# Performance work log

Measured on AMD Instinct MI355X. Metric: run time of the kernel, lower is better.

Reference implementation:

```python
import jax, jax.numpy as jnp
import numpy as np

HID = 4096; H = 128; P = 64; N = 128; G = 8; K = 4; CH = 128
INTER = H * P                      # 8192
CONV_DIM = INTER + 2 * G * N       # 10240
PROJ = INTER + CONV_DIM + H        # 18560
EPS = 1e-5


def segsum(x):
    # stable segment-sum: out[..., i, j] = sum_{j < k <= i} x[..., k]; -inf above diagonal
    T = x.shape[-1]
    xe = jnp.repeat(x[..., None], T, axis=-1)          # [..., i, j] = x[..., i]
    strict = jnp.tril(jnp.ones((T, T), bool), -1)
    s = jnp.cumsum(jnp.where(strict, xe, 0.0), axis=-2)
    keep = jnp.tril(jnp.ones((T, T), bool), 0)
    return jnp.where(keep, s, -jnp.inf)


def setup_inputs() -> dict:
    key = jax.random.key(0)
    ks = jax.random.split(key, 6)
    b, L = 2, 2048
    hidden_states = jax.random.normal(ks[0], (b, L, HID), jnp.float32)
    in_proj_w = jax.random.normal(ks[1], (PROJ, HID), jnp.float32) * (HID ** -0.5)
    conv_w = jax.random.normal(ks[2], (CONV_DIM, 1, K), jnp.float32) * 0.2
    conv_b = jax.random.normal(ks[3], (CONV_DIM,), jnp.float32) * 0.02
    dt_bias = jnp.ones((H,), jnp.float32)
    A_log = jnp.log(jnp.arange(1, H + 1, dtype=jnp.float32))
    D = jnp.ones((H,), jnp.float32)
    norm_weight = jnp.ones((INTER,), jnp.float32)
    out_proj_w = jax.random.normal(ks[4], (HID, INTER), jnp.float32) * (INTER ** -0.5)
    return dict(hidden_states=hidden_states, in_proj_w=in_proj_w, conv_w=conv_w, conv_b=conv_b,
                dt_bias=dt_bias, A_log=A_log, D=D, norm_weight=norm_weight, out_proj_w=out_proj_w)


def _mamba2(hidden_states, in_proj_w, conv_w, conv_b, dt_bias, A_log, D, norm_weight, out_proj_w):
    b, L, _ = hidden_states.shape
    nchunk = L // CH  # seq_len chosen to be a multiple of chunk_size (pad_size = 0)

    # in_proj and split into gate | conv path (x,B,C) | dt
    proj = hidden_states @ in_proj_w.T
    gate, hBC, dt = jnp.split(proj, [INTER, INTER + CONV_DIM], axis=-1)

    # causal depthwise conv1d (padding k-1, truncate) + SiLU
    xp = jnp.pad(hBC.transpose(0, 2, 1), ((0, 0), (0, 0), (K - 1, 0)))
    xc = jax.lax.conv_general_dilated(xp, conv_w, (1,), 'VALID',
                                      feature_group_count=CONV_DIM,
                                      dimension_numbers=('NCW', 'OIW', 'NCW'))
    hBC = jax.nn.silu((xc + conv_b[None, :, None]).transpose(0, 2, 1))
    hs, Bx, Cx = jnp.split(hBC, [INTER, INTER + G * N], axis=-1)

    A = -jnp.exp(A_log)                      # [H]
    dt = jax.nn.softplus(dt + dt_bias)       # time_step_limit = (0, inf) -> clamp is no-op

    hs = hs.reshape(b, L, H, P)
    rep = H // G
    Bm = jnp.tile(Bx.reshape(b, L, G, N), (1, 1, rep, 1))   # matches torch .repeat
    Cm = jnp.tile(Cx.reshape(b, L, G, N), (1, 1, rep, 1))

    D_res = D[None, None, :, None] * hs      # [b,L,H,P]

    # discretize and chunk
    X = (hs * dt[..., None]).reshape(b, nchunk, CH, H, P)
    A_dt = (A[None, None, :] * dt).reshape(b, nchunk, CH, H).transpose(0, 3, 1, 2)  # [b,H,c,l]
    Bc = Bm.reshape(b, nchunk, CH, H, N)
    Cc = Cm.reshape(b, nchunk, CH, H, N)
    A_cs = jnp.cumsum(A_dt, axis=-1)

    # 1. intra-chunk (diagonal blocks)
    Lmat = jnp.exp(segsum(A_dt))                              # [b,H,c,l,s]
    Gm = jnp.einsum('bclhn,bcshn->bclsh', Cc, Bc)
    M = Gm * Lmat.transpose(0, 2, 3, 4, 1)                    # [b,c,l,s,H]
    Y_diag = jnp.einsum('bclsh,bcshp->bclhp', M, X)

    # 2. per-chunk states
    decay_states = jnp.exp(A_cs[..., -1:] - A_cs)             # [b,H,c,l]
    B_decay = Bc * decay_states.transpose(0, 2, 3, 1)[..., None]
    states = jnp.einsum('bclhn,bclhp->bchpn', B_decay, X)     # [b,c,H,P,N]

    # 3. inter-chunk recurrence
    states = jnp.concatenate([jnp.zeros_like(states[:, :1]), states], axis=1)
    A_last = jnp.pad(A_cs[..., -1], ((0, 0), (0, 0), (1, 0)))  # [b,H,c+1]
    decay_chunk = jnp.exp(segsum(A_last)).transpose(0, 3, 2, 1)  # [b,c+1,c+1,H]
    new_states = jnp.einsum('bzjh,bzhpn->bjhpn', decay_chunk, states)
    prev_states = new_states[:, :-1]                           # [b,c,H,P,N]

    # 4. state -> output
    sdo = jnp.exp(A_cs).transpose(0, 2, 3, 1)                  # [b,c,l,H]
    Y_off = jnp.einsum('bclhn,bchpn->bclhp', Cc, prev_states) * sdo[..., None]

    y = (Y_diag + Y_off).reshape(b, L, H, P) + D_res
    scan_out = y.reshape(b, L, INTER)

    # gated group RMSNorm (norm_before_gate=False: gate first, then group-RMS)
    xg = scan_out * jax.nn.silu(gate)
    xr = xg.reshape(b, L, G, INTER // G)
    xr = xr * jax.lax.rsqrt(jnp.mean(xr * xr, axis=-1, keepdims=True) + EPS)
    normed = xr.reshape(b, L, INTER) * norm_weight

    return normed @ out_proj_w.T


def reference(hidden_states, in_proj_w, conv_w, conv_b, dt_bias, A_log, D, norm_weight, out_proj_w):
    return _mamba2(hidden_states, in_proj_w, conv_w, conv_b, dt_bias, A_log, D, norm_weight, out_proj_w)
```

## Files before the change

kernel.cpp:

```cpp
#include <hip/hip_runtime.h>

#define NH 128
#define PD 64
#define NSD 128
#define NG 8
#define CHK 128
#define HIDD 4096
#define INTER_D 8192
#define CONV_D 10240
#define PROJ_D 18560
#define SEQ 2048
#define ROWS 4096
#define NCH 16

typedef __attribute__((ext_vector_type(8))) short bf16x8;
typedef __attribute__((ext_vector_type(4))) float f32x4;

__device__ __forceinline__ unsigned short f2bf(float f) {
  unsigned int u = __float_as_uint(f);
  u += 0x7FFF + ((u >> 16) & 1);
  return (unsigned short)(u >> 16);
}
__device__ __forceinline__ float bf2f(unsigned short s) {
  return __uint_as_float(((unsigned int)s) << 16);
}

__device__ __forceinline__ void gld16(const unsigned short* g, unsigned short* l) {
  __builtin_amdgcn_global_load_lds(
      (__attribute__((address_space(1))) const void*)g,
      (__attribute__((address_space(3))) void*)l, 16, 0, 0);
}

#define BAR() __builtin_amdgcn_s_barrier()
#define SCHED() __builtin_amdgcn_sched_barrier(0)
#define VMCNT(n) asm volatile("s_waitcnt vmcnt(" #n ")" ::: "memory")

__device__ __forceinline__ bf16x8 ldsfrag(const unsigned short* slot, int row, int kslot) {
  int byte = row * 128 + (((kslot ^ (row & 7)) << 4));
  return *(const bf16x8*)((const char*)slot + byte);
}

__global__ __launch_bounds__(256) void cvt_kernel(const float* __restrict__ in,
                                                  unsigned short* __restrict__ out,
                                                  size_t n) {
  size_t i = ((size_t)blockIdx.x * 256 + threadIdx.x) * 4;
  if (i < n) {
    float4 f = *(const float4*)(in + i);
    ushort4 o;
    o.x = f2bf(f.x); o.y = f2bf(f.y); o.z = f2bf(f.z); o.w = f2bf(f.w);
    *(ushort4*)(out + i) = o;
  }
}

template <int OUT_BF16>
__global__ __launch_bounds__(512, 2) void gemm256(const unsigned short* __restrict__ A,
                                                  const unsigned short* __restrict__ B,
                                                  unsigned short* __restrict__ outb,
                                                  float* __restrict__ outf,
                                                  int Nreal, int Ks, int Kl, int koff) {
  __shared__ unsigned short lds[8][8192];
  int tid = threadIdx.x, l = tid & 63, w = tid >> 6;
  int wm = w >> 2, wn = w & 3;
  int il = l & 15, fog = l >> 4;
  int bid = blockIdx.x;
  int xcd = bid & 7, local = bid >> 3;
  int mt = xcd * 2 + (local & 1), nt = local >> 1;
  const unsigned short* Abase = A + (size_t)mt * 256 * Ks + koff;
  const unsigned short* Bbase = B + (size_t)nt * 256 * Ks + koff;
  int NT = Kl >> 6;

  f32x4 acc[2][2][4][2];
#pragma unroll
  for (int a = 0; a < 2; ++a)
#pragma unroll
    for (int b = 0; b < 2; ++b)
#pragma unroll
      for (int m = 0; m < 4; ++m)
#pragma unroll
        for (int n = 0; n < 2; ++n) acc[a][b][m][n] = (f32x4){0.f, 0.f, 0.f, 0.f};

  auto STG = [&](int tt, int ty) {
    int tc = tt < NT ? tt : NT - 1;
    const unsigned short* g = ((ty & 1) ? Bbase : Abase) + (size_t)((ty >> 1) * 128) * Ks + tc * 64;
    unsigned short* sp = (unsigned short*)lds[(tt & 1) * 4 + ty];
#pragma unroll
    for (int j = 0; j < 2; ++j) {
      int row = (j * 8 + w) * 8 + (l >> 3);
      int scol = ((l & 7) ^ (row & 7)) * 8;
      gld16(g + (size_t)row * Ks + scol, sp + (j * 8 + w) * 512);
    }
  };

#define LDA(SLOT)                                          \
  _Pragma("unroll") for (int mi = 0; mi < 4; ++mi)         \
  _Pragma("unroll") for (int kk = 0; kk < 2; ++kk)         \
      av[mi][kk] = ldsfrag(SLOT, wm * 64 + mi * 16 + il, kk * 4 + fog);
#define LDB(QN, SLOT)                                      \
  _Pragma("unroll") for (int ni = 0; ni < 2; ++ni)         \
  _Pragma("unroll") for (int kk = 0; kk < 2; ++kk)         \
      bv[QN][ni][kk] = ldsfrag(SLOT, wn * 32 + ni * 16 + il, kk * 4 + fog);
#define MFMA_PH(QM, QN)                                    \
  _Pragma("unroll") for (int mi = 0; mi < 4; ++mi)         \
  _Pragma("unroll") for (int ni = 0; ni < 2; ++ni)         \
  _Pragma("unroll") for (int kk = 0; kk < 2; ++kk)         \
      acc[QM][QN][mi][ni] = __builtin_amdgcn_mfma_f32_16x16x32_bf16( \
          av[mi][kk], bv[QN][ni][kk], acc[QM][QN][mi][ni], 0, 0, 0);

  STG(0, 0); STG(0, 1); STG(0, 3); STG(0, 2);
  VMCNT(2);
  BAR(); SCHED();

  for (int t = 0; t < NT; ++t) {
    const unsigned short* sA0 = lds[(t & 1) * 4 + 0];
    const unsigned short* sB0 = lds[(t & 1) * 4 + 1];
    const unsigned short* sA1 = lds[(t & 1) * 4 + 2];
    const unsigned short* sB1 = lds[(t & 1) * 4 + 3];
    bf16x8 av[4][2], bv[2][2][2];
    LDA(sA0); LDB(0, sB0); LDB(1, sB1);
    STG(t + 1, 0); STG(t + 1, 1);
    BAR();
    __builtin_amdgcn_s_setprio(1);
    MFMA_PH(0, 0);
    __builtin_amdgcn_s_setprio(0);
    VMCNT(4);
    BAR(); SCHED();
    STG(t + 1, 3);
    __builtin_amdgcn_s_setprio(1);
    MFMA_PH(0, 1);
    __builtin_amdgcn_s_setprio(0);
    BAR();
    LDA(sA1);
    STG(t + 1, 2);
    BAR();
    __builtin_amdgcn_s_setprio(1);
    MFMA_PH(1, 0);
    __builtin_amdgcn_s_setprio(0);
    BAR();
    __builtin_amdgcn_s_setprio(1);
    MFMA_PH(1, 1);
    __builtin_amdgcn_s_setprio(0);
    VMCNT(2);
    BAR(); SCHED();
  }
  VMCNT(0);

  int rl = (l >> 4) * 4;
#pragma unroll
  for (int qm = 0; qm < 2; ++qm)
#pragma unroll
    for (int qn = 0; qn < 2; ++qn)
#pragma unroll
      for (int mi = 0; mi < 4; ++mi)
#pragma unroll
        for (int ni = 0; ni < 2; ++ni) {
          int grow = mt * 256 + qm * 128 + wm * 64 + mi * 16 + rl;
          int gcol = nt * 256 + qn * 128 + wn * 32 + ni * 16 + il;
          if (!OUT_BF16 || gcol < Nreal) {
#pragma unroll
            for (int r = 0; r < 4; ++r) {
              float v = acc[qm][qn][mi][ni][r];
              if (OUT_BF16)
                outb[(size_t)(grow + r) * Nreal + gcol] = f2bf(v);
              else
                outf[(size_t)(grow + r) * Nreal + gcol] = v;
            }
          }
        }
#undef LDA
#undef LDB
#undef MFMA_PH
}

__global__ __launch_bounds__(128) void dts_kernel(const unsigned short* __restrict__ proj,
                                                  const float* __restrict__ dt_bias,
                                                  const float* __restrict__ A_log,
                                                  float* __restrict__ dtg,
                                                  float* __restrict__ acsg) {
  int bc = blockIdx.x;
  int h = threadIdx.x;
  int b = bc >> 4, c = bc & 15;
  float A = -__expf(A_log[h]);
  float bias = dt_bias[h];
  float cum = 0.f;
  int row0 = b * SEQ + c * CHK;
#pragma unroll 4
  for (int ll = 0; ll < CHK; ++ll) {
    float x = bf2f(proj[(size_t)(row0 + ll) * PROJ_D + (PROJ_D - NH) + h]) + bias;
    float d = (x > 20.f) ? x : log1pf(expf(x));
    dtg[(size_t)(row0 + ll) * NH + h] = d;
    cum += A * d;
    acsg[(((size_t)bc * NH) + h) * CHK + ll] = cum;
  }
}

__global__ __launch_bounds__(256) void conv_kernel(const unsigned short* __restrict__ proj,
                                                   const float* __restrict__ cw,
                                                   const float* __restrict__ cb,
                                                   unsigned short* __restrict__ xbc) {
  int ch = blockIdx.x * 256 + threadIdx.x;
  int row = blockIdx.y;
  int b = row >> 11, ll = row & 2047;
  float acc = cb[ch];
#pragma unroll
  for (int k = 0; k < 4; ++k) {
    int l2 = ll - 3 + k;
    if (l2 >= 0)
      acc += bf2f(proj[(size_t)(b * SEQ + l2) * PROJ_D + INTER_D + ch]) * cw[ch * 4 + k];
  }
  float s = acc / (1.f + __expf(-acc));
  xbc[(size_t)row * CONV_D + ch] = f2bf(s);
}

__global__ __launch_bounds__(256) void e1b_kernel(const unsigned short* __restrict__ xbc,
                                                  const float* __restrict__ dtg,
                                                  const float* __restrict__ acsg,
                                                  float* __restrict__ states) {
  int bid = blockIdx.x;
  int h = bid & 127, c = (bid >> 7) & 15, b = bid >> 11;
  int g = h & 7;
  int row0 = b * SEQ + c * CHK;
  __shared__ __align__(16) char smem[52736];
  unsigned short* XT = (unsigned short*)smem;
  unsigned short* BdT = (unsigned short*)(smem + 17408);
  float* Acs = (float*)(smem + 52224);
  int tid = threadIdx.x, lane = tid & 63, wv = tid >> 6;
  int fo = (lane >> 4) * 8, il = lane & 15, rl = (lane >> 4) * 4;
  if (tid < 128) Acs[tid] = acsg[(((size_t)(b * NCH + c) * NH) + h) * CHK + tid];
  __syncthreads();
#pragma unroll
  for (int j = 0; j < 4; ++j) {
    int q = tid + j * 256;
    int ll = q >> 3, p0 = (q & 7) * 8;
    int row = row0 + ll;
    float dtv = dtg[(size_t)row * NH + h];
    int4 raw = *(const int4*)(xbc + (size_t)row * CONV_D + h * PD + p0);
    unsigned short* u = (unsigned short*)&raw;
#pragma unroll
    for (int e = 0; e < 8; ++e) XT[(p0 + e) * 136 + ll] = f2bf(bf2f(u[e]) * dtv);
  }
#pragma unroll
  for (int j = 0; j < 8; ++j) {
    int q = tid + j * 256;
    int ll = q >> 4, n0 = (q & 15) * 8;
    float dec = __expf(Acs[CHK - 1] - Acs[ll]);
    int4 raw = *(const int4*)(xbc + (size_t)(row0 + ll) * CONV_D + INTER_D + g * NSD + n0);
    unsigned short* u = (unsigned short*)&raw;
#pragma unroll
    for (int e = 0; e < 8; ++e) BdT[(n0 + e) * 136 + ll] = f2bf(bf2f(u[e]) * dec);
  }
  __syncthreads();
  f32x4 st[8];
#pragma unroll
  for (int i = 0; i < 8; ++i) st[i] = (f32x4){0.f, 0.f, 0.f, 0.f};
#pragma unroll
  for (int ks = 0; ks < 4; ++ks) {
    bf16x8 a = *(const bf16x8*)&XT[(wv * 16 + il) * 136 + ks * 32 + fo];
#pragma unroll
    for (int ni = 0; ni < 8; ++ni) {
      bf16x8 bb = *(const bf16x8*)&BdT[(ni * 16 + il) * 136 + ks * 32 + fo];
      st[ni] = __builtin_amdgcn_mfma_f32_16x16x32_bf16(a, bb, st[ni], 0, 0, 0);
    }
  }
  size_t base = ((size_t)(b * NH + h) * NCH + c) * (PD * NSD);
#pragma unroll
  for (int ni = 0; ni < 8; ++ni) {
    int n = ni * 16 + il;
#pragma unroll
    for (int r = 0; r < 4; ++r) {
      int p = wv * 16 + rl + r;
      states[base + p * NSD + n] = st[ni][r];
    }
  }
}

__global__ __launch_bounds__(256) void e2_kernel(const float* __restrict__ acsg,
                                                 const float* __restrict__ states,
                                                 unsigned short* __restrict__ prevs) {
  int bid = blockIdx.x;
  int bh = bid >> 2, pg = bid & 3;
  int b = bh >> 7;
  int t = threadIdx.x;
  float S[8];
#pragma unroll
  for (int j = 0; j < 8; ++j) S[j] = 0.f;
  for (int c = 0; c < NCH; ++c) {
    float alast = acsg[(((size_t)((b * NCH + c) * NH) + (bh & 127))) * CHK + (CHK - 1)];
    float dec = __expf(alast);
    size_t base = ((size_t)bh * NCH + c) * (PD * NSD) + (size_t)pg * 2048;
#pragma unroll
    for (int j = 0; j < 8; ++j) {
      size_t e = base + (size_t)j * 256 + t;
      float v = states[e];
      prevs[e] = f2bf(S[j]);
      S[j] = S[j] * dec + v;
    }
  }
}

__global__ __launch_bounds__(512) void e13_kernel(const unsigned short* __restrict__ xbc,
                                                  const float* __restrict__ dtg,
                                                  const float* __restrict__ acsg,
                                                  const unsigned short* __restrict__ prevs,
                                                  const float* __restrict__ Dp,
                                                  unsigned short* __restrict__ ybh) {
  int bid = blockIdx.x;
  int h = bid & 127, c = (bid >> 7) & 15, b = bid >> 11;
  int g = h & 7;
  int row0 = b * SEQ + c * CHK;
  __shared__ __align__(16) char smem[70144];
  unsigned short* Cst = (unsigned short*)smem;
  unsigned short* Bst = (unsigned short*)(smem + 10240);
  unsigned short* Mt = (unsigned short*)smem;
  unsigned short* Ct = (unsigned short*)smem;
  unsigned short* XT = (unsigned short*)(smem + 34816);
  unsigned short* Sp = (unsigned short*)(smem + 52224);
  float* Acs = (float*)(smem + 69632);
  int tid = threadIdx.x, lane = tid & 63, wv = tid >> 6;
  int fo = (lane >> 4) * 8, il = lane & 15, rl = (lane >> 4) * 4;
  if (tid < 128) Acs[tid] = acsg[(((size_t)(b * NCH + c) * NH) + h) * CHK + tid];

  f32x4 gm[8];
#pragma unroll
  for (int i = 0; i < 8; ++i) gm[i] = (f32x4){0.f, 0.f, 0.f, 0.f};
  int srow = tid >> 2, scol = (tid & 3) * 8;
  for (int kc = 0; kc < 4; ++kc) {
    __syncthreads();
    *(int4*)(Cst + srow * 40 + scol) =
        *(const int4*)(xbc + (size_t)(row0 + srow) * CONV_D + INTER_D + NG * NSD + g * NSD + kc * 32 + scol);
    *(int4*)(Bst + srow * 40 + scol) =
        *(const int4*)(xbc + (size_t)(row0 + srow) * CONV_D + INTER_D + g * NSD + kc * 32 + scol);
    __syncthreads();
    bf16x8 a = *(const bf16x8*)&Cst[(wv * 16 + il) * 40 + fo];
#pragma unroll
    for (int ni = 0; ni < 8; ++ni) {
      bf16x8 bb = *(const bf16x8*)&Bst[(ni * 16 + il) * 40 + fo];
      gm[ni] = __builtin_amdgcn_mfma_f32_16x16x32_bf16(a, bb, gm[ni], 0, 0, 0);
    }
  }
  __syncthreads();
#pragma unroll
  for (int ni = 0; ni < 8; ++ni) {
    int s = ni * 16 + il;
#pragma unroll
    for (int r = 0; r < 4; ++r) {
      int ll = wv * 16 + rl + r;
      float v = (s <= ll) ? gm[ni][r] * __expf(Acs[ll] - Acs[s]) : 0.f;
      Mt[ll * 136 + s] = f2bf(v);
    }
  }
#pragma unroll
  for (int j = 0; j < 2; ++j) {
    int q = tid + j * 512;
    int ll = q >> 3, p0 = (q & 7) * 8;
    int row = row0 + ll;
    float dtv = dtg[(size_t)row * NH + h];
    int4 raw = *(const int4*)(xbc + (size_t)row * CONV_D + h * PD + p0);
    unsigned short* u = (unsigned short*)&raw;
#pragma unroll
    for (int e = 0; e < 8; ++e) XT[(p0 + e) * 136 + ll] = f2bf(bf2f(u[e]) * dtv);
  }
  size_t sbase = ((size_t)(b * NH + h) * NCH + c) * (PD * NSD);
#pragma unroll
  for (int j = 0; j < 2; ++j) {
    int q = tid + j * 512;
    int p = q >> 4, n0 = (q & 15) * 8;
    *(int4*)(Sp + p * 136 + n0) = *(const int4*)(prevs + sbase + p * NSD + n0);
  }
  __syncthreads();
  f32x4 yd[4];
#pragma unroll
  for (int i = 0; i < 4; ++i) yd[i] = (f32x4){0.f, 0.f, 0.f, 0.f};
#pragma unroll
  for (int ks = 0; ks < 4; ++ks) {
    bf16x8 a = *(const bf16x8*)&Mt[(wv * 16 + il) * 136 + ks * 32 + fo];
#pragma unroll
    for (int pi = 0; pi < 4; ++pi) {
      bf16x8 bb = *(const bf16x8*)&XT[(pi * 16 + il) * 136 + ks * 32 + fo];
      yd[pi] = __builtin_amdgcn_mfma_f32_16x16x32_bf16(a, bb, yd[pi], 0, 0, 0);
    }
  }
  __syncthreads();
#pragma unroll
  for (int j = 0; j < 4; ++j) {
    int q = tid + j * 512;
    int ll = q >> 4, n0 = (q & 15) * 8;
    *(int4*)(Ct + ll * 136 + n0) =
        *(const int4*)(xbc + (size_t)(row0 + ll) * CONV_D + INTER_D + NG * NSD + g * NSD + n0);
  }
  __syncthreads();
  f32x4 yo[4];
#pragma unroll
  for (int i = 0; i < 4; ++i) yo[i] = (f32x4){0.f, 0.f, 0.f, 0.f};
#pragma unroll
  for (int ks = 0; ks < 4; ++ks) {
    bf16x8 a = *(const bf16x8*)&Ct[(wv * 16 + il) * 136 + ks * 32 + fo];
#pragma unroll
    for (int pi = 0; pi < 4; ++pi) {
      bf16x8 bb = *(const bf16x8*)&Sp[(pi * 16 + il) * 136 + ks * 32 + fo];
      yo[pi] = __builtin_amdgcn_mfma_f32_16x16x32_bf16(a, bb, yo[pi], 0, 0, 0);
    }
  }
  float dv = Dp[h];
#pragma unroll
  for (int pi = 0; pi < 4; ++pi) {
    int p = pi * 16 + il;
#pragma unroll
    for (int r = 0; r < 4; ++r) {
      int ll = wv * 16 + rl + r;
      int row = row0 + ll;
      float hsv = bf2f(xbc[(size_t)row * CONV_D + h * PD + p]);
      ybh[(size_t)row * INTER_D + h * PD + p] =
          f2bf(yd[pi][r] + yo[pi][r] * __expf(Acs[ll]) + dv * hsv);
    }
  }
}

__global__ __launch_bounds__(256) void fnorm_kernel(const unsigned short* __restrict__ ybh,
                                                    const unsigned short* __restrict__ proj,
                                                    const float* __restrict__ nw,
                                                    unsigned short* __restrict__ normed) {
  int row = blockIdx.x >> 3;
  int gg = blockIdx.x & 7;
  int t = threadIdx.x;
  float v[4];
  float ss = 0.f;
#pragma unroll
  for (int j = 0; j < 4; ++j) {
    int ch = gg * 1024 + j * 256 + t;
    float val = bf2f(ybh[(size_t)row * INTER_D + ch]);
    float gt = bf2f(proj[(size_t)row * PROJ_D + ch]);
    val *= gt / (1.f + __expf(-gt));
    v[j] = val;
    ss += val * val;
  }
  __shared__ float sred[256];
  sred[t] = ss;
  __syncthreads();
  for (int ofs = 128; ofs > 0; ofs >>= 1) {
    if (t < ofs) sred[t] += sred[t + ofs];
    __syncthreads();
  }
  float rms = rsqrtf(sred[0] / 1024.f + 1e-5f);
#pragma unroll
  for (int j = 0; j < 4; ++j) {
    int ch = gg * 1024 + j * 256 + t;
    normed[(size_t)row * INTER_D + ch] = f2bf(v[j] * rms * nw[ch]);
  }
}

extern "C" void kernel_launch(void* const* d_in, const int* in_sizes, int n_in,
                              void* d_out, int out_size, void* d_ws, size_t ws_size,
                              hipStream_t stream) {
  (void)in_sizes; (void)n_in; (void)out_size; (void)ws_size;
  const float* hs = (const float*)d_in[0];
  const float* w1 = (const float*)d_in[1];
  const float* cw = (const float*)d_in[2];
  const float* cb = (const float*)d_in[3];
  const float* dtb = (const float*)d_in[4];
  const float* alog = (const float*)d_in[5];
  const float* Dp = (const float*)d_in[6];
  const float* nw = (const float*)d_in[7];
  const float* w2 = (const float*)d_in[8];
  float* out = (float*)d_out;
  char* ws = (char*)d_ws;

  unsigned short* hsb = (unsigned short*)(ws);
  unsigned short* w1b = (unsigned short*)(ws + 33554432);
  unsigned short* w2b = (unsigned short*)(ws + 186646528);
  unsigned short* proj = (unsigned short*)(ws + 253755392);
  unsigned short* xbc = (unsigned short*)(ws + 405798912);
  float* dtg = (float*)(ws + 489684992);
  float* acsg = (float*)(ws + 491782144);
  float* states = (float*)(ws + 493879296);
  unsigned short* prevs = (unsigned short*)(ws + 628097024);
  unsigned short* ybh = (unsigned short*)(ws + 695205888);
  unsigned short* normed = (unsigned short*)(ws);

  cvt_kernel<<<dim3(16384), dim3(256), 0, stream>>>(hs, hsb, (size_t)ROWS * HIDD);
  cvt_kernel<<<dim3(74240), dim3(256), 0, stream>>>(w1, w1b, (size_t)PROJ_D * HIDD);
  cvt_kernel<<<dim3(32768), dim3(256), 0, stream>>>(w2, w2b, (size_t)HIDD * INTER_D);

  gemm256<1><<<dim3(16 * 73), dim3(512), 0, stream>>>(hsb, w1b, proj, nullptr,
                                                      PROJ_D, HIDD, HIDD, 0);
  dts_kernel<<<dim3(32), dim3(128), 0, stream>>>(proj, dtb, alog, dtg, acsg);
  conv_kernel<<<dim3(40, 4096), dim3(256), 0, stream>>>(proj, cw, cb, xbc);
  e1b_kernel<<<dim3(4096), dim3(256), 0, stream>>>(xbc, dtg, acsg, states);
  e2_kernel<<<dim3(1024), dim3(256), 0, stream>>>(acsg, states, prevs);
  e13_kernel<<<dim3(4096), dim3(512), 0, stream>>>(xbc, dtg, acsg, prevs, Dp, ybh);
  fnorm_kernel<<<dim3(32768), dim3(256), 0, stream>>>(ybh, proj, nw, normed);
  gemm256<0><<<dim3(16 * 16), dim3(512), 0, stream>>>(normed, w2b, nullptr, out,
                                                      HIDD, INTER_D, INTER_D, 0);
}
```

Baseline: 1.436 ms.

## Store chunk states in bf16 and fuse off-diagonal MMA reusing C fragments

Measured after the change: 1.410 ms. Within noise of the previous version (-1.8%).

```diff
diff --git a/kernel.cpp b/kernel.cpp
--- a/kernel.cpp
+++ b/kernel.cpp
@@ -214,7 +214,7 @@
 __global__ __launch_bounds__(256) void e1b_kernel(const unsigned short* __restrict__ xbc,
                                                   const float* __restrict__ dtg,
                                                   const float* __restrict__ acsg,
-                                                  float* __restrict__ states) {
+                                                  unsigned short* __restrict__ states16) {
   int bid = blockIdx.x;
   int h = bid & 127, c = (bid >> 7) & 15, b = bid >> 11;
   int g = h & 7;
@@ -268,13 +268,13 @@
 #pragma unroll
     for (int r = 0; r < 4; ++r) {
       int p = wv * 16 + rl + r;
-      states[base + p * NSD + n] = st[ni][r];
+      states16[base + p * NSD + n] = f2bf(st[ni][r]);
     }
   }
 }
 
 __global__ __launch_bounds__(256) void e2_kernel(const float* __restrict__ acsg,
-                                                 const float* __restrict__ states,
+                                                 const unsigned short* __restrict__ states16,
                                                  unsigned short* __restrict__ prevs) {
   int bid = blockIdx.x;
   int bh = bid >> 2, pg = bid & 3;
@@ -290,7 +290,7 @@
 #pragma unroll
     for (int j = 0; j < 8; ++j) {
       size_t e = base + (size_t)j * 256 + t;
-      float v = states[e];
+      float v = bf2f(states16[e]);
       prevs[e] = f2bf(S[j]);
       S[j] = S[j] * dec + v;
     }
@@ -311,7 +311,6 @@
   unsigned short* Cst = (unsigned short*)smem;
   unsigned short* Bst = (unsigned short*)(smem + 10240);
   unsigned short* Mt = (unsigned short*)smem;
-  unsigned short* Ct = (unsigned short*)smem;
   unsigned short* XT = (unsigned short*)(smem + 34816);
   unsigned short* Sp = (unsigned short*)(smem + 52224);
   float* Acs = (float*)(smem + 69632);
@@ -322,7 +321,9 @@
   f32x4 gm[8];
 #pragma unroll
   for (int i = 0; i < 8; ++i) gm[i] = (f32x4){0.f, 0.f, 0.f, 0.f};
+  bf16x8 cf[4];
   int srow = tid >> 2, scol = (tid & 3) * 8;
+#pragma unroll
   for (int kc = 0; kc < 4; ++kc) {
     __syncthreads();
     *(int4*)(Cst + srow * 40 + scol) =
@@ -331,6 +332,7 @@
         *(const int4*)(xbc + (size_t)(row0 + srow) * CONV_D + INTER_D + g * NSD + kc * 32 + scol);
     __syncthreads();
     bf16x8 a = *(const bf16x8*)&Cst[(wv * 16 + il) * 40 + fo];
+    cf[kc] = a;
 #pragma unroll
     for (int ni = 0; ni < 8; ++ni) {
       bf16x8 bb = *(const bf16x8*)&Bst[(ni * 16 + il) * 40 + fo];
@@ -367,37 +369,21 @@
     *(int4*)(Sp + p * 136 + n0) = *(const int4*)(prevs + sbase + p * NSD + n0);
   }
   __syncthreads();
-  f32x4 yd[4];
-#pragma unroll
-  for (int i = 0; i < 4; ++i) yd[i] = (f32x4){0.f, 0.f, 0.f, 0.f};
+  f32x4 yd[4], yo[4];
+#pragma unroll
+  for (int i = 0; i < 4; ++i) {
+    yd[i] = (f32x4){0.f, 0.f, 0.f, 0.f};
+    yo[i] = (f32x4){0.f, 0.f, 0.f, 0.f};
+  }
 #pragma unroll
   for (int ks = 0; ks < 4; ++ks) {
     bf16x8 a = *(const bf16x8*)&Mt[(wv * 16 + il) * 136 + ks * 32 + fo];
 #pragma unroll
     for (int pi = 0; pi < 4; ++pi) {
       bf16x8 bb = *(const bf16x8*)&XT[(pi * 16 + il) * 136 + ks * 32 + fo];
+      bf16x8 sb = *(const bf16x8*)&Sp[(pi * 16 + il) * 136 + ks * 32 + fo];
       yd[pi] = __builtin_amdgcn_mfma_f32_16x16x32_bf16(a, bb, yd[pi], 0, 0, 0);
-    }
-  }
-  __syncthreads();
-#pragma unroll
-  for (int j = 0; j < 4; ++j) {
-    int q = tid + j * 512;
-    int ll = q >> 4, n0 = (q & 15) * 8;
-    *(int4*)(Ct + ll * 136 + n0) =
-        *(const int4*)(xbc + (size_t)(row0 + ll) * CONV_D + INTER_D + NG * NSD + g * NSD + n0);
-  }
-  __syncthreads();
-  f32x4 yo[4];
-#pragma unroll
-  for (int i = 0; i < 4; ++i) yo[i] = (f32x4){0.f, 0.f, 0.f, 0.f};
-#pragma unroll
-  for (int ks = 0; ks < 4; ++ks) {
-    bf16x8 a = *(const bf16x8*)&Ct[(wv * 16 + il) * 136 + ks * 32 + fo];
-#pragma unroll
-    for (int pi = 0; pi < 4; ++pi) {
-      bf16x8 bb = *(const bf16x8*)&Sp[(pi * 16 + il) * 136 + ks * 32 + fo];
-      yo[pi] = __builtin_amdgcn_mfma_f32_16x16x32_bf16(a, bb, yo[pi], 0, 0, 0);
+      yo[pi] = __builtin_amdgcn_mfma_f32_16x16x32_bf16(cf[ks], sb, yo[pi], 0, 0, 0);
     }
   }
   float dv = Dp[h];
@@ -471,9 +457,9 @@
   unsigned short* xbc = (unsigned short*)(ws + 405798912);
   float* dtg = (float*)(ws + 489684992);
   float* acsg = (float*)(ws + 491782144);
-  float* states = (float*)(ws + 493879296);
-  unsigned short* prevs = (unsigned short*)(ws + 628097024);
-  unsigned short* ybh = (unsigned short*)(ws + 695205888);
+  unsigned short* states16 = (unsigned short*)(ws + 493879296);
+  unsigned short* prevs = (unsigned short*)(ws + 560988160);
+  unsigned short* ybh = (unsigned short*)(ws + 628097024);
   unsigned short* normed = (unsigned short*)(ws);
 
   cvt_kernel<<<dim3(16384), dim3(256), 0, stream>>>(hs, hsb, (size_t)ROWS * HIDD);
@@ -484,8 +470,8 @@
                                                       PROJ_D, HIDD, HIDD, 0);
   dts_kernel<<<dim3(32), dim3(128), 0, stream>>>(proj, dtb, alog, dtg, acsg);
   conv_kernel<<<dim3(40, 4096), dim3(256), 0, stream>>>(proj, cw, cb, xbc);
-  e1b_kernel<<<dim3(4096), dim3(256), 0, stream>>>(xbc, dtg, acsg, states);
-  e2_kernel<<<dim3(1024), dim3(256), 0, stream>>>(acsg, states, prevs);
+  e1b_kernel<<<dim3(4096), dim3(256), 0, stream>>>(xbc, dtg, acsg, states16);
+  e2_kernel<<<dim3(1024), dim3(256), 0, stream>>>(acsg, states16, prevs);
   e13_kernel<<<dim3(4096), dim3(512), 0, stream>>>(xbc, dtg, acsg, prevs, Dp, ybh);
   fnorm_kernel<<<dim3(32768), dim3(256), 0, stream>>>(ybh, proj, nw, normed);
   gemm256<0><<<dim3(16 * 16), dim3(512), 0, stream>>>(normed, w2b, nullptr, out,
```
